# Kernel optimization log

Measured on AMD Instinct MI355X. Metric: run time of the kernel, lower is better.

Reference implementation:

```python
import jax, jax.numpy as jnp
import numpy as np

B, C, H, W = 8, 256, 128, 128
G = 32            # n_groups
CPG = C // G      # channels per group = 8
K = 3             # adaptive spatial kernel and final conv kernel
OUT = 256         # out_channels of final conv
EPS = 1e-5
DN = ('NCHW', 'OIHW', 'NCHW')


def setup_inputs() -> dict:
    key = jax.random.key(0)
    ks = jax.random.split(key, 6)
    x = jax.random.normal(ks[0], (B, C, H, W), jnp.float32)
    w_spatial = jax.random.normal(ks[1], (B, C, CPG, K, K), jnp.float32) * 0.05
    w_pointwise = jax.random.normal(ks[2], (B, C, CPG, 1, 1), jnp.float32) * 0.05
    bias = jax.random.normal(ks[3], (B, C), jnp.float32) * 0.05
    # learned params of the final (static) conv
    conv_w = jax.random.normal(ks[4], (OUT, C, K, K), jnp.float32) * 0.05
    conv_b = jax.random.normal(ks[5], (OUT,), jnp.float32) * 0.05
    return {'x': x, 'w_spatial': w_spatial, 'w_pointwise': w_pointwise,
            'bias': bias, 'conv_w': conv_w, 'conv_b': conv_b}


def _ada_single(x, ws, wp, b):
    # x: [C,H,W]; ws: [C,CPG,K,K]; wp: [C,CPG,1,1]; b: [C]
    pad = (K - 1) // 2
    xp = jnp.pad(x, ((0, 0), (pad, pad), (pad, pad)), mode='reflect')
    # grouped spatial conv (channel-preserving)
    y = jax.lax.conv_general_dilated(
        xp[None], ws, (1, 1), 'VALID',
        dimension_numbers=DN, feature_group_count=G)[0]      # [C,H,W]
    # grouped 1x1 conv as per-group small matmul
    yg = y.reshape(G, CPG, H, W)
    wg = wp[:, :, 0, 0].reshape(G, CPG, CPG)                 # [G, out/g, in/g]
    z = jnp.einsum('goi,gihw->gohw', wg, yg).reshape(C, H, W)
    return z + b[:, None, None]


def reference(x, w_spatial, w_pointwise, bias, conv_w, conv_b):
    # instance norm (no affine), biased variance as in F.instance_norm
    mean = x.mean(axis=(2, 3), keepdims=True)
    var = x.var(axis=(2, 3), keepdims=True)
    xn = (x - mean) * jax.lax.rsqrt(var + EPS)
    # per-sample adaptive depthwise-separable conv
    y = jax.vmap(_ada_single)(xn, w_spatial, w_pointwise, bias)  # [B,C,H,W]
    # final static conv, reflect padding (ceil,floor) = (1,1) for k=3
    yp = jnp.pad(y, ((0, 0), (0, 0), (1, 1), (1, 1)), mode='reflect')
    out = jax.lax.conv_general_dilated(yp, conv_w, (1, 1), 'VALID',
                                       dimension_numbers=DN)
    return out + conv_b[None, :, None, None]
```

## Files before the change

### kernel.cpp

```cpp
#include <hip/hip_runtime.h>
#include <stdint.h>
#include <stddef.h>


typedef __attribute__((ext_vector_type(8))) short   s16x8;
typedef __attribute__((ext_vector_type(4))) float   f32x4;

#define NB   8
#define NC   256
#define NH   128
#define NW   128
#define NG   32
#define CPG  8
#define NOUT 256
#define HWPLANE (NH*NW)

__device__ __forceinline__ unsigned short f2bf(float f) {
    union { float f; unsigned u; } v; v.f = f;
    unsigned u = v.u;
    u += 0x7fffu + ((u >> 16) & 1u);
    return (unsigned short)(u >> 16);
}

__device__ __forceinline__ int refl128(int i) {
    return i < 0 ? 1 : (i > 127 ? 126 : i);
}

__device__ __forceinline__ void async_load16(const void* g, void* l) {
    __builtin_amdgcn_global_load_lds(
        (const __attribute__((address_space(1))) unsigned int*)g,
        (__attribute__((address_space(3))) unsigned int*)l,
        16, 0, 0);
}

__global__ __launch_bounds__(256) void stats_k(const float* __restrict__ x,
                                               float* __restrict__ stats) {
    int bc = blockIdx.x, t = threadIdx.x;
    const float4* p = (const float4*)(x + (size_t)bc * HWPLANE);
    float s = 0.f, q = 0.f;
#pragma unroll
    for (int k = 0; k < 16; ++k) {
        float4 v = p[k * 256 + t];
        s += v.x + v.y + v.z + v.w;
        q += v.x * v.x + v.y * v.y + v.z * v.z + v.w * v.w;
    }
    __shared__ float ss[256], sq[256];
    ss[t] = s; sq[t] = q;
    __syncthreads();
    for (int o = 128; o > 0; o >>= 1) {
        if (t < o) { ss[t] += ss[t + o]; sq[t] += sq[t + o]; }
        __syncthreads();
    }
    if (t == 0) {
        float mean = ss[0] * (1.f / HWPLANE);
        float var  = sq[0] * (1.f / HWPLANE) - mean * mean;
        stats[bc * 2]     = mean;
        stats[bc * 2 + 1] = rsqrtf(var + 1e-5f);
    }
}

__global__ __launch_bounds__(256) void weff_k(const float* __restrict__ wsp,
                                              const float* __restrict__ wpw,
                                              float* __restrict__ weff) {
    int tid = blockIdx.x * 256 + threadIdx.x;
    int oc = tid & 7;
    int q  = tid >> 3;
    int t  = q % 9;
    int q2 = q / 9;
    int ic = q2 & 7;
    int bg = q2 >> 3;
    float acc = 0.f;
#pragma unroll
    for (int j = 0; j < 8; ++j)
        acc += wpw[(bg * 8 + oc) * 8 + j] * wsp[((bg * 8 + j) * 8 + ic) * 9 + t];
    weff[(size_t)((bg * 8 + ic) * 9 + t) * 8 + oc] = acc;
}

__global__ __launch_bounds__(256) void repack_k(const float* __restrict__ cw,
                                                unsigned short* __restrict__ wtT) {
    int tid = blockIdx.x * 256 + threadIdx.x;
    int c = tid & 255;
    int o = (tid >> 8) & 255;
    int t = tid >> 16;
    float v = cw[(size_t)(o * NC + c) * 9 + t];
    wtT[((size_t)t * NOUT + o) * NC + c] = f2bf(v);
}

__global__ __launch_bounds__(256) void ada_k(const float* __restrict__ x,
                                             const float* __restrict__ stats,
                                             const float* __restrict__ weff,
                                             const float* __restrict__ bias,
                                             unsigned short* __restrict__ z) {
    __shared__ float sx[CPG][10][NW];
    const int bx = blockIdx.x;
    const int ht = bx & 15;
    const int g  = (bx >> 4) & 31;
    const int b  = bx >> 9;
    const int h0 = ht * 8;

#pragma unroll
    for (int it = 0; it < 10; ++it) {
        int p   = it * 256 + threadIdx.x;
        int ic  = p / 320;
        int rem = p - ic * 320;
        int row = rem >> 5;
        int w4  = rem & 31;
        int cg  = g * 8 + ic;
        float mean = stats[(b * NC + cg) * 2];
        float rstd = stats[(b * NC + cg) * 2 + 1];
        int rr = refl128(h0 - 1 + row);
        const float4* xp4 = (const float4*)(x + (size_t)(b * NC + cg) * HWPLANE + rr * NW);
        float4 v = xp4[w4];
        float4 n = { (v.x - mean) * rstd, (v.y - mean) * rstd,
                     (v.z - mean) * rstd, (v.w - mean) * rstd };
        *(float4*)&sx[ic][row][w4 * 4] = n;
    }
    __syncthreads();

    const int w  = threadIdx.x & 127;
    const int hq = threadIdx.x >> 7;

    const float* wbase = weff + (size_t)(b * NG + g) * 576;
    const float* bp    = bias + b * NC + g * 8;

    float acc[4][8];
#pragma unroll
    for (int r = 0; r < 4; ++r)
#pragma unroll
        for (int oc = 0; oc < 8; ++oc) acc[r][oc] = bp[oc];

#pragma unroll
    for (int ic = 0; ic < CPG; ++ic) {
#pragma unroll
        for (int dw = 0; dw < 3; ++dw) {
            int wc = w + dw - 1;
            wc = wc < 0 ? 1 : (wc > 127 ? 126 : wc);
            float xr[6];
#pragma unroll
            for (int rr = 0; rr < 6; ++rr) xr[rr] = sx[ic][hq * 4 + rr][wc];
#pragma unroll
            for (int dh = 0; dh < 3; ++dh) {
                const float* wv = wbase + (ic * 9 + dh * 3 + dw) * 8;
#pragma unroll
                for (int r = 0; r < 4; ++r)
#pragma unroll
                    for (int oc = 0; oc < 8; ++oc)
                        acc[r][oc] += wv[oc] * xr[r + dh];
            }
        }
    }

#pragma unroll
    for (int r = 0; r < 4; ++r) {
        int h = h0 + hq * 4 + r;
        unsigned short ob[8];
#pragma unroll
        for (int oc = 0; oc < 8; ++oc) ob[oc] = f2bf(acc[r][oc]);
        uint4 pk;
        pk.x = (unsigned)ob[0] | ((unsigned)ob[1] << 16);
        pk.y = (unsigned)ob[2] | ((unsigned)ob[3] << 16);
        pk.z = (unsigned)ob[4] | ((unsigned)ob[5] << 16);
        pk.w = (unsigned)ob[6] | ((unsigned)ob[7] << 16);
        *(uint4*)(z + (size_t)(((b * NG + g) * NH + h) * NW + w) * 8) = pk;
    }
}

__global__ __launch_bounds__(256, 3) void final_k(const unsigned short* __restrict__ z,
                                                  const unsigned short* __restrict__ wtT,
                                                  const float* __restrict__ cb,
                                                  float* __restrict__ out) {
    __shared__ s16x8 sAv[1024];
    __shared__ s16x8 sBv[2][1024];

    const int id = blockIdx.x;
    const int b  = id & 7;
    const int jb = id >> 3;
    const int nb = jb & 1;
    const int h  = jb >> 1;

    const int tid  = threadIdx.x;
    const int wv   = tid >> 6;
    const int lane = tid & 63;
    const int l15  = lane & 15;
    const int quad = lane >> 4;
    const int mo   = (wv & 1) << 6;
    const int nol  = (wv >> 1) << 6;
    const int n0   = (nb << 7) + nol;

    int srcB[4], ldsoff[4];
#pragma unroll
    for (int it = 0; it < 4; ++it) {
        int ch  = it * 256 + tid;
        int row = ch >> 3, cp = ch & 7;
        srcB[it]   = row * 512 + ((cp ^ (row & 7)) << 4);
        ldsoff[it] = it * 256 + wv * 64;
    }

    int srcA[4];
#pragma unroll
    for (int it = 0; it < 4; ++it) {
        int ch = it * 256 + tid;
        int gq = ch >> 7, wslot = ch & 127;
        srcA[it] = gq * 262144 + ((wslot ^ (gq & 7)) << 4);
    }

    int aoff[3][4][2];
#pragma unroll
    for (int dw = 0; dw < 3; ++dw)
#pragma unroll
        for (int i = 0; i < 4; ++i) {
            int w_ = refl128(mo + 16 * i + l15 + dw - 1);
#pragma unroll
            for (int kk = 0; kk < 2; ++kk) {
                int gq = kk * 4 + quad;
                aoff[dw][i][kk] = gq * 128 + (w_ ^ (gq & 7));
            }
        }
    int boff[4][2];
#pragma unroll
    for (int j = 0; j < 4; ++j) {
        int oc_l = nol + 16 * j + l15;
#pragma unroll
        for (int kk = 0; kk < 2; ++kk)
            boff[j][kk] = oc_l * 8 + ((kk * 4 + quad) ^ (oc_l & 7));
    }

    const char* zb = (const char*)z + (size_t)b * (NG * NH * NW * CPG * 2);
    const char* zr[3];
#pragma unroll
    for (int dh = 0; dh < 3; ++dh)
        zr[dh] = zb + (size_t)refl128(h + dh - 1) * (NW * CPG * 2);
    const char* wt = (const char*)wtT + nb * 65536;

    auto stageA = [&](const char* g) {
#pragma unroll
        for (int it = 0; it < 4; ++it)
            async_load16(g + srcA[it], (void*)(sAv + ldsoff[it]));
    };
    auto stageB = [&](const char* g, int bsel) {
#pragma unroll
        for (int it = 0; it < 4; ++it)
            async_load16(g + srcB[it], (void*)(sBv[bsel] + ldsoff[it]));
    };

    f32x4 acc[4][4] = {};

    auto compute = [&](const int (&ao)[4][2], int bsel) {
        const s16x8* bbase = sBv[bsel];
#pragma unroll
        for (int kk = 0; kk < 2; ++kk) {
            s16x8 av[4], bv[4];
#pragma unroll
            for (int i = 0; i < 4; ++i) av[i] = sAv[ao[i][kk]];
#pragma unroll
            for (int j = 0; j < 4; ++j) bv[j] = bbase[boff[j][kk]];
#pragma unroll
            for (int i = 0; i < 4; ++i)
#pragma unroll
                for (int j = 0; j < 4; ++j)
                    acc[i][j] = __builtin_amdgcn_mfma_f32_16x16x32_bf16(
                        av[i], bv[j], acc[i][j], 0, 0, 0);
        }
    };

    int buf = 0;
    stageA(zr[0]);
    stageB(wt, 0);
    __syncthreads();

    for (int sc = 0; sc < 12; ++sc) {
        const int dh = sc >> 2, kc = sc & 3;
        const char* bt = wt + (size_t)(dh * 3) * 131072 + kc * 128;
        stageB(bt + 131072, buf ^ 1);
        compute(aoff[0], buf);
        __syncthreads(); buf ^= 1;
        stageB(bt + 262144, buf ^ 1);
        compute(aoff[1], buf);
        __syncthreads(); buf ^= 1;
        compute(aoff[2], buf);
        __syncthreads();
        if (sc < 11) {
            const int sn = sc + 1, dhn = sn >> 2, kcn = sn & 3;
            stageA(zr[dhn] + (size_t)kcn * 2097152);
            stageB(wt + (size_t)(dhn * 3) * 131072 + kcn * 128, buf ^ 1);
            __syncthreads();
        }
        buf ^= 1;
    }

#pragma unroll
    for (int j = 0; j < 4; ++j) {
        int oc = n0 + 16 * j + l15;
        float bvl = cb[oc];
#pragma unroll
        for (int i = 0; i < 4; ++i) {
            int w0 = mo + 16 * i + quad * 4;
            float* dst = out + (((size_t)(b * NOUT + oc) * NH + h) * NW + w0);
            f32x4 v = acc[i][j];
            float4 o4 = { v[0] + bvl, v[1] + bvl, v[2] + bvl, v[3] + bvl };
            *(float4*)dst = o4;
        }
    }
}

extern "C" void kernel_launch(void* const* d_in, const int* in_sizes, int n_in,
                              void* d_out, int out_size, void* d_ws, size_t ws_size,
                              hipStream_t stream) {
    const float* x   = (const float*)d_in[0];
    const float* wsp = (const float*)d_in[1];
    const float* wpw = (const float*)d_in[2];
    const float* bia = (const float*)d_in[3];
    const float* cw  = (const float*)d_in[4];
    const float* cb  = (const float*)d_in[5];
    float* out = (float*)d_out;

    char* ws = (char*)d_ws;
    float*          stats = (float*)ws;
    float*          weff  = (float*)(ws + 16384);
    unsigned short* wtT   = (unsigned short*)(ws + 606208);
    unsigned short* z     = (unsigned short*)(ws + 1785856);

    stats_k <<<NB * NC, 256, 0, stream>>>(x, stats);
    weff_k  <<<576,     256, 0, stream>>>(wsp, wpw, weff);
    repack_k<<<2304,    256, 0, stream>>>(cw, wtT);
    ada_k   <<<NB * NG * (NH / 8), 256, 0, stream>>>(x, stats, weff, bia, z);
    final_k <<<NB * NH * 2,  256, 0, stream>>>(z, wtT, cb, out);
}
```

Baseline: 428.2 us.

## Load conv weights directly to registers and double-buffer input tile in LDS

The final conv kernel stops staging weight (B) tiles through shared memory. Each wave now reads its B fragments from global memory straight into registers, while the activation (A) tile is double-buffered in LDS so the next tile loads during compute. This cuts the barriers per chunk from several to one. The A LDS layout changes to a w-major swizzle, MFMA sections get raised scheduling priority, and the occupancy hint in launch_bounds is dropped. The cost is more register pressure and repeated global/L2 reads of weights per wave, which may lower occupancy.

After: 611.0 us. +42.7%, slower.

```diff
diff --git a/kernel.cpp b/kernel.cpp
--- a/kernel.cpp
+++ b/kernel.cpp
@@ -165,12 +165,11 @@
     }
 }
 
-__global__ __launch_bounds__(256, 3) void final_k(const unsigned short* __restrict__ z,
-                                                  const unsigned short* __restrict__ wtT,
-                                                  const float* __restrict__ cb,
-                                                  float* __restrict__ out) {
-    __shared__ s16x8 sAv[1024];
-    __shared__ s16x8 sBv[2][1024];
+__global__ __launch_bounds__(256) void final_k(const unsigned short* __restrict__ z,
+                                               const unsigned short* __restrict__ wtT,
+                                               const float* __restrict__ cb,
+                                               float* __restrict__ out) {
+    __shared__ s16x8 sAv[2][1024];
 
     const int id = blockIdx.x;
     const int b  = id & 7;
@@ -187,21 +186,14 @@
     const int nol  = (wv >> 1) << 6;
     const int n0   = (nb << 7) + nol;
 
-    int srcB[4], ldsoff[4];
-#pragma unroll
-    for (int it = 0; it < 4; ++it) {
-        int ch  = it * 256 + tid;
-        int row = ch >> 3, cp = ch & 7;
-        srcB[it]   = row * 512 + ((cp ^ (row & 7)) << 4);
-        ldsoff[it] = it * 256 + wv * 64;
-    }
-
-    int srcA[4];
+    int srcA[4], ldsoff[4];
 #pragma unroll
     for (int it = 0; it < 4; ++it) {
         int ch = it * 256 + tid;
-        int gq = ch >> 7, wslot = ch & 127;
-        srcA[it] = gq * 262144 + ((wslot ^ (gq & 7)) << 4);
+        int w_ = ch >> 3, s = ch & 7;
+        int gq = s ^ (w_ & 7);
+        srcA[it]   = gq * 262144 + w_ * 16;
+        ldsoff[it] = it * 256 + wv * 64;
     }
 
     int aoff[3][4][2];
@@ -213,16 +205,17 @@
 #pragma unroll
             for (int kk = 0; kk < 2; ++kk) {
                 int gq = kk * 4 + quad;
-                aoff[dw][i][kk] = gq * 128 + (w_ ^ (gq & 7));
+                aoff[dw][i][kk] = w_ * 8 + (gq ^ (w_ & 7));
             }
         }
-    int boff[4][2];
+
+    int boffr[4][2];
 #pragma unroll
     for (int j = 0; j < 4; ++j) {
         int oc_l = nol + 16 * j + l15;
 #pragma unroll
         for (int kk = 0; kk < 2; ++kk)
-            boff[j][kk] = oc_l * 8 + ((kk * 4 + quad) ^ (oc_l & 7));
+            boffr[j][kk] = oc_l * 512 + (kk * 4 + quad) * 16;
     }
 
     const char* zb = (const char*)z + (size_t)b * (NG * NH * NW * CPG * 2);
@@ -232,59 +225,59 @@
         zr[dh] = zb + (size_t)refl128(h + dh - 1) * (NW * CPG * 2);
     const char* wt = (const char*)wtT + nb * 65536;
 
-    auto stageA = [&](const char* g) {
+    auto stageA = [&](const char* g, int sel) {
 #pragma unroll
         for (int it = 0; it < 4; ++it)
-            async_load16(g + srcA[it], (void*)(sAv + ldsoff[it]));
+            async_load16(g + srcA[it], (void*)(sAv[sel] + ldsoff[it]));
     };
-    auto stageB = [&](const char* g, int bsel) {
-#pragma unroll
-        for (int it = 0; it < 4; ++it)
-            async_load16(g + srcB[it], (void*)(sBv[bsel] + ldsoff[it]));
+    auto loadB = [&](const char* bt, s16x8 (&bv)[4][2]) {
+#pragma unroll
+        for (int j = 0; j < 4; ++j)
+#pragma unroll
+            for (int kk = 0; kk < 2; ++kk)
+                bv[j][kk] = *(const s16x8*)(bt + boffr[j][kk]);
     };
 
     f32x4 acc[4][4] = {};
 
-    auto compute = [&](const int (&ao)[4][2], int bsel) {
-        const s16x8* bbase = sBv[bsel];
+    auto compute = [&](const int (&ao)[4][2], const s16x8 (&bv)[4][2], int sel) {
+        const s16x8* abase = sAv[sel];
+        __builtin_amdgcn_s_setprio(1);
 #pragma unroll
         for (int kk = 0; kk < 2; ++kk) {
-            s16x8 av[4], bv[4];
-#pragma unroll
-            for (int i = 0; i < 4; ++i) av[i] = sAv[ao[i][kk]];
-#pragma unroll
-            for (int j = 0; j < 4; ++j) bv[j] = bbase[boff[j][kk]];
+            s16x8 av[4];
+#pragma unroll
+            for (int i = 0; i < 4; ++i) av[i] = abase[ao[i][kk]];
 #pragma unroll
             for (int i = 0; i < 4; ++i)
 #pragma unroll
                 for (int j = 0; j < 4; ++j)
                     acc[i][j] = __builtin_amdgcn_mfma_f32_16x16x32_bf16(
-                        av[i], bv[j], acc[i][j], 0, 0, 0);
-        }
+                        av[i], bv[j][kk], acc[i][j], 0, 0, 0);
+        }
+        __builtin_amdgcn_s_setprio(0);
     };
 
     int buf = 0;
-    stageA(zr[0]);
-    stageB(wt, 0);
+    stageA(zr[0], 0);
     __syncthreads();
 
     for (int sc = 0; sc < 12; ++sc) {
         const int dh = sc >> 2, kc = sc & 3;
-        const char* bt = wt + (size_t)(dh * 3) * 131072 + kc * 128;
-        stageB(bt + 131072, buf ^ 1);
-        compute(aoff[0], buf);
-        __syncthreads(); buf ^= 1;
-        stageB(bt + 262144, buf ^ 1);
-        compute(aoff[1], buf);
-        __syncthreads(); buf ^= 1;
-        compute(aoff[2], buf);
+        const char* bt0 = wt + (size_t)(dh * 3) * 131072 + kc * 128;
+
+        s16x8 bvA[4][2], bvB[4][2];
+        loadB(bt0, bvA);
+        if (sc < 11) {
+            const int sn = sc + 1;
+            stageA(zr[sn >> 2] + (size_t)(sn & 3) * 2097152, buf ^ 1);
+        }
+        loadB(bt0 + 131072, bvB);
+        compute(aoff[0], bvA, buf);
+        loadB(bt0 + 262144, bvA);
+        compute(aoff[1], bvB, buf);
+        compute(aoff[2], bvA, buf);
         __syncthreads();
-        if (sc < 11) {
-            const int sn = sc + 1, dhn = sn >> 2, kcn = sn & 3;
-            stageA(zr[dhn] + (size_t)kcn * 2097152);
-            stageB(wt + (size_t)(dhn * 3) * 131072 + kcn * 128, buf ^ 1);
-            __syncthreads();
-        }
         buf ^= 1;
     }
 
```

## Compute two output rows per block in final conv to share weight tiles

Applied to the files above, without the earlier changes.

The final conv kernel now uses 512-thread blocks that each produce two output rows instead of one. Staged weight (B) tiles in LDS are shared across both rows, which halves weight traffic per output, and the A tile is restaged as two rows with a new swizzle. MFMA sections are also wrapped in s_setprio to favour compute waves. The cost is a larger LDS footprint, half as many blocks, and the loss of the explicit 3-block occupancy hint.

Result: slower. 496.8 us (+16.0%).

```diff
diff --git a/kernel.cpp b/kernel.cpp
--- a/kernel.cpp
+++ b/kernel.cpp
@@ -165,43 +165,49 @@
     }
 }
 
-__global__ __launch_bounds__(256, 3) void final_k(const unsigned short* __restrict__ z,
-                                                  const unsigned short* __restrict__ wtT,
-                                                  const float* __restrict__ cb,
-                                                  float* __restrict__ out) {
-    __shared__ s16x8 sAv[1024];
+__global__ __launch_bounds__(512) void final_k(const unsigned short* __restrict__ z,
+                                               const unsigned short* __restrict__ wtT,
+                                               const float* __restrict__ cb,
+                                               float* __restrict__ out) {
+    __shared__ s16x8 sAv[2048];
     __shared__ s16x8 sBv[2][1024];
 
     const int id = blockIdx.x;
     const int b  = id & 7;
     const int jb = id >> 3;
     const int nb = jb & 1;
-    const int h  = jb >> 1;
+    const int ht = jb >> 1;
+    const int h0 = ht * 2;
 
     const int tid  = threadIdx.x;
     const int wv   = tid >> 6;
     const int lane = tid & 63;
     const int l15  = lane & 15;
     const int quad = lane >> 4;
-    const int mo   = (wv & 1) << 6;
-    const int nol  = (wv >> 1) << 6;
+    const int wsub = wv & 3;
+    const int hrow = wsub >> 1;
+    const int wo   = (wsub & 1) << 6;
+    const int nol  = (wv >> 2) << 6;
     const int n0   = (nb << 7) + nol;
 
-    int srcB[4], ldsoff[4];
+    int srcA[4], ldsA[4];
 #pragma unroll
     for (int it = 0; it < 4; ++it) {
-        int ch  = it * 256 + tid;
-        int row = ch >> 3, cp = ch & 7;
-        srcB[it]   = row * 512 + ((cp ^ (row & 7)) << 4);
-        ldsoff[it] = it * 256 + wv * 64;
-    }
-
-    int srcA[4];
-#pragma unroll
-    for (int it = 0; it < 4; ++it) {
-        int ch = it * 256 + tid;
-        int gq = ch >> 7, wslot = ch & 127;
-        srcA[it] = gq * 262144 + ((wslot ^ (gq & 7)) << 4);
+        int ch = it * 512 + tid;
+        int cw = (ch >> 3) & 127;
+        int s  = ch & 7;
+        int gq = s ^ (cw & 7);
+        srcA[it] = gq * 262144 + cw * 16;
+        ldsA[it] = it * 512 + wv * 64;
+    }
+
+    int srcB[2], ldsB[2];
+#pragma unroll
+    for (int it = 0; it < 2; ++it) {
+        int ch = it * 512 + tid;
+        int oc = ch >> 3, cp = ch & 7;
+        srcB[it] = oc * 512 + ((cp ^ (oc & 7)) << 4);
+        ldsB[it] = it * 512 + wv * 64;
     }
 
     int aoff[3][4][2];
@@ -209,11 +215,11 @@
     for (int dw = 0; dw < 3; ++dw)
 #pragma unroll
         for (int i = 0; i < 4; ++i) {
-            int w_ = refl128(mo + 16 * i + l15 + dw - 1);
+            int w_ = refl128(wo + 16 * i + l15 + dw - 1);
 #pragma unroll
             for (int kk = 0; kk < 2; ++kk) {
                 int gq = kk * 4 + quad;
-                aoff[dw][i][kk] = gq * 128 + (w_ ^ (gq & 7));
+                aoff[dw][i][kk] = hrow * 1024 + w_ * 8 + (gq ^ (w_ & 7));
             }
         }
     int boff[4][2];
@@ -226,27 +232,29 @@
     }
 
     const char* zb = (const char*)z + (size_t)b * (NG * NH * NW * CPG * 2);
-    const char* zr[3];
-#pragma unroll
-    for (int dh = 0; dh < 3; ++dh)
-        zr[dh] = zb + (size_t)refl128(h + dh - 1) * (NW * CPG * 2);
+    const char* zrow[4];
+#pragma unroll
+    for (int r = 0; r < 4; ++r)
+        zrow[r] = zb + (size_t)refl128(h0 + r - 1) * (NW * CPG * 2);
     const char* wt = (const char*)wtT + nb * 65536;
 
-    auto stageA = [&](const char* g) {
-#pragma unroll
-        for (int it = 0; it < 4; ++it)
-            async_load16(g + srcA[it], (void*)(sAv + ldsoff[it]));
+    auto stageA = [&](const char* rp0, const char* rp1) {
+        async_load16(rp0 + srcA[0], (void*)(sAv + ldsA[0]));
+        async_load16(rp0 + srcA[1], (void*)(sAv + ldsA[1]));
+        async_load16(rp1 + srcA[2], (void*)(sAv + ldsA[2]));
+        async_load16(rp1 + srcA[3], (void*)(sAv + ldsA[3]));
     };
     auto stageB = [&](const char* g, int bsel) {
 #pragma unroll
-        for (int it = 0; it < 4; ++it)
-            async_load16(g + srcB[it], (void*)(sBv[bsel] + ldsoff[it]));
+        for (int it = 0; it < 2; ++it)
+            async_load16(g + srcB[it], (void*)(sBv[bsel] + ldsB[it]));
     };
 
     f32x4 acc[4][4] = {};
 
     auto compute = [&](const int (&ao)[4][2], int bsel) {
         const s16x8* bbase = sBv[bsel];
+        __builtin_amdgcn_s_setprio(1);
 #pragma unroll
         for (int kk = 0; kk < 2; ++kk) {
             s16x8 av[4], bv[4];
@@ -261,10 +269,11 @@
                     acc[i][j] = __builtin_amdgcn_mfma_f32_16x16x32_bf16(
                         av[i], bv[j], acc[i][j], 0, 0, 0);
         }
+        __builtin_amdgcn_s_setprio(0);
     };
 
     int buf = 0;
-    stageA(zr[0]);
+    stageA(zrow[0], zrow[1]);
     stageB(wt, 0);
     __syncthreads();
 
@@ -281,20 +290,22 @@
         __syncthreads();
         if (sc < 11) {
             const int sn = sc + 1, dhn = sn >> 2, kcn = sn & 3;
-            stageA(zr[dhn] + (size_t)kcn * 2097152);
+            const size_t ko = (size_t)kcn * 2097152;
+            stageA(zrow[dhn] + ko, zrow[dhn + 1] + ko);
             stageB(wt + (size_t)(dhn * 3) * 131072 + kcn * 128, buf ^ 1);
             __syncthreads();
         }
         buf ^= 1;
     }
 
+    const int h = h0 + hrow;
 #pragma unroll
     for (int j = 0; j < 4; ++j) {
         int oc = n0 + 16 * j + l15;
         float bvl = cb[oc];
 #pragma unroll
         for (int i = 0; i < 4; ++i) {
-            int w0 = mo + 16 * i + quad * 4;
+            int w0 = wo + 16 * i + quad * 4;
             float* dst = out + (((size_t)(b * NOUT + oc) * NH + h) * NW + w0);
             f32x4 v = acc[i][j];
             float4 o4 = { v[0] + bvl, v[1] + bvl, v[2] + bvl, v[3] + bvl };
@@ -324,5 +335,5 @@
     weff_k  <<<576,     256, 0, stream>>>(wsp, wpw, weff);
     repack_k<<<2304,    256, 0, stream>>>(cw, wtT);
     ada_k   <<<NB * NG * (NH / 8), 256, 0, stream>>>(x, stats, weff, bia, z);
-    final_k <<<NB * NH * 2,  256, 0, stream>>>(z, wtT, cb, out);
-}
+    final_k <<<NB * NH * 2 / 2, 512, 0, stream>>>(z, wtT, cb, out);
+}
```

## Compute adaptive grouped conv with bf16 MFMA and change z layout swizzle

Applied to the files above, without the earlier changes.

The adaptive grouped 3x3+1x1 conv moves from scalar fp32 FMAs to bf16 MFMA 16x16x32. The fused effective weights are pre-packed into per-lane fragments, with 9 taps padded to 12 and 8 output channels padded to 16. Each block now normalizes a 34-row bf16 tile for 32 output rows, and the final conv's A-load swizzle is changed to match the new LDS addressing. This cuts the VALU cost of the ada stage but wastes half the MFMA outputs and lowers the normalized input to bf16 before the first conv. It also drops the occupancy hint on final_k.

Measured after the change: 447.9 us. +4.6%, slower.

```diff
diff --git a/kernel.cpp b/kernel.cpp
--- a/kernel.cpp
+++ b/kernel.cpp
@@ -59,21 +59,41 @@
     }
 }
 
-__global__ __launch_bounds__(256) void weff_k(const float* __restrict__ wsp,
-                                              const float* __restrict__ wpw,
-                                              float* __restrict__ weff) {
+__global__ __launch_bounds__(256) void wfrag_k(const float* __restrict__ wsp,
+                                               const float* __restrict__ wpw,
+                                               const float* __restrict__ bias,
+                                               unsigned short* __restrict__ wfrag,
+                                               float* __restrict__ bias16) {
     int tid = blockIdx.x * 256 + threadIdx.x;
-    int oc = tid & 7;
-    int q  = tid >> 3;
-    int t  = q % 9;
-    int q2 = q / 9;
-    int ic = q2 & 7;
-    int bg = q2 >> 3;
-    float acc = 0.f;
-#pragma unroll
-    for (int j = 0; j < 8; ++j)
-        acc += wpw[(bg * 8 + oc) * 8 + j] * wsp[((bg * 8 + j) * 8 + ic) * 9 + t];
-    weff[(size_t)((bg * 8 + ic) * 9 + t) * 8 + oc] = acc;
+    if (tid < 49152) {
+        int lane = tid & 63;
+        int kw   = (tid >> 6) % 3;
+        int bg   = tid / 192;
+        int oc   = lane & 15;
+        int tap  = kw * 4 + (lane >> 4);
+        unsigned short fr[8];
+#pragma unroll
+        for (int e = 0; e < 8; ++e) {
+            float v = 0.f;
+            if (tap < 9 && oc < 8) {
+#pragma unroll
+                for (int j = 0; j < 8; ++j)
+                    v += wpw[(bg * 8 + oc) * 8 + j] *
+                         wsp[((bg * 8 + j) * 8 + e) * 9 + tap];
+            }
+            fr[e] = f2bf(v);
+        }
+        uint4 pk;
+        pk.x = (unsigned)fr[0] | ((unsigned)fr[1] << 16);
+        pk.y = (unsigned)fr[2] | ((unsigned)fr[3] << 16);
+        pk.z = (unsigned)fr[4] | ((unsigned)fr[5] << 16);
+        pk.w = (unsigned)fr[6] | ((unsigned)fr[7] << 16);
+        *(uint4*)(wfrag + (size_t)((bg * 3 + kw) * 64 + lane) * 8) = pk;
+    } else {
+        int t2 = tid - 49152;
+        int bg = t2 >> 4, j = t2 & 15;
+        bias16[bg * 16 + j] = (j < 8) ? bias[bg * 8 + j] : 0.f;
+    }
 }
 
 __global__ __launch_bounds__(256) void repack_k(const float* __restrict__ cw,
@@ -88,87 +108,95 @@
 
 __global__ __launch_bounds__(256) void ada_k(const float* __restrict__ x,
                                              const float* __restrict__ stats,
-                                             const float* __restrict__ weff,
-                                             const float* __restrict__ bias,
+                                             const unsigned short* __restrict__ wfrag,
+                                             const float* __restrict__ bias16,
                                              unsigned short* __restrict__ z) {
-    __shared__ float sx[CPG][10][NW];
-    const int bx = blockIdx.x;
-    const int ht = bx & 15;
-    const int g  = (bx >> 4) & 31;
-    const int b  = bx >> 9;
-    const int h0 = ht * 8;
-
-#pragma unroll
-    for (int it = 0; it < 10; ++it) {
-        int p   = it * 256 + threadIdx.x;
-        int ic  = p / 320;
-        int rem = p - ic * 320;
-        int row = rem >> 5;
-        int w4  = rem & 31;
-        int cg  = g * 8 + ic;
-        float mean = stats[(b * NC + cg) * 2];
-        float rstd = stats[(b * NC + cg) * 2 + 1];
-        int rr = refl128(h0 - 1 + row);
-        const float4* xp4 = (const float4*)(x + (size_t)(b * NC + cg) * HWPLANE + rr * NW);
-        float4 v = xp4[w4];
-        float4 n = { (v.x - mean) * rstd, (v.y - mean) * rstd,
-                     (v.z - mean) * rstd, (v.w - mean) * rstd };
-        *(float4*)&sx[ic][row][w4 * 4] = n;
+    __shared__ s16x8 tile[34 * 128];
+    const int id = blockIdx.x;
+    const int b  = id & 7;
+    const int g  = (id >> 3) & 31;
+    const int q  = id >> 8;
+    const int bg = b * 32 + g;
+    const int h0 = q * 32;
+
+    const int tid  = threadIdx.x;
+    const int lane = tid & 63;
+    const int wv   = tid >> 6;
+    const int l15  = lane & 15;
+    const int quad = lane >> 4;
+
+    float mean[8], rstd[8];
+#pragma unroll
+    for (int ic = 0; ic < 8; ++ic) {
+        mean[ic] = stats[(bg * 8 + ic) * 2];
+        rstd[ic] = stats[(bg * 8 + ic) * 2 + 1];
+    }
+
+    const float* xg = x + (size_t)bg * 8 * HWPLANE;
+#pragma unroll
+    for (int it = 0; it < 17; ++it) {
+        int slot = it * 256 + tid;
+        int row  = slot >> 7;
+        int w    = slot & 127;
+        int gr   = refl128(h0 - 1 + row);
+        const float* xp = xg + gr * NW + w;
+        unsigned short u[8];
+#pragma unroll
+        for (int ic = 0; ic < 8; ++ic)
+            u[ic] = f2bf((xp[(size_t)ic * HWPLANE] - mean[ic]) * rstd[ic]);
+        uint4 pk;
+        pk.x = (unsigned)u[0] | ((unsigned)u[1] << 16);
+        pk.y = (unsigned)u[2] | ((unsigned)u[3] << 16);
+        pk.z = (unsigned)u[4] | ((unsigned)u[5] << 16);
+        pk.w = (unsigned)u[6] | ((unsigned)u[7] << 16);
+        *(uint4*)&tile[slot] = pk;
     }
     __syncthreads();
 
-    const int w  = threadIdx.x & 127;
-    const int hq = threadIdx.x >> 7;
-
-    const float* wbase = weff + (size_t)(b * NG + g) * 576;
-    const float* bp    = bias + b * NC + g * 8;
-
-    float acc[4][8];
-#pragma unroll
-    for (int r = 0; r < 4; ++r)
-#pragma unroll
-        for (int oc = 0; oc < 8; ++oc) acc[r][oc] = bp[oc];
-
-#pragma unroll
-    for (int ic = 0; ic < CPG; ++ic) {
-#pragma unroll
-        for (int dw = 0; dw < 3; ++dw) {
-            int wc = w + dw - 1;
-            wc = wc < 0 ? 1 : (wc > 127 ? 126 : wc);
-            float xr[6];
-#pragma unroll
-            for (int rr = 0; rr < 6; ++rr) xr[rr] = sx[ic][hq * 4 + rr][wc];
-#pragma unroll
-            for (int dh = 0; dh < 3; ++dh) {
-                const float* wv = wbase + (ic * 9 + dh * 3 + dw) * 8;
-#pragma unroll
-                for (int r = 0; r < 4; ++r)
-#pragma unroll
-                    for (int oc = 0; oc < 8; ++oc)
-                        acc[r][oc] += wv[oc] * xr[r + dh];
-            }
-        }
-    }
-
-#pragma unroll
-    for (int r = 0; r < 4; ++r) {
-        int h = h0 + hq * 4 + r;
-        unsigned short ob[8];
-#pragma unroll
-        for (int oc = 0; oc < 8; ++oc) ob[oc] = f2bf(acc[r][oc]);
-        uint4 pk;
-        pk.x = (unsigned)ob[0] | ((unsigned)ob[1] << 16);
-        pk.y = (unsigned)ob[2] | ((unsigned)ob[3] << 16);
-        pk.z = (unsigned)ob[4] | ((unsigned)ob[5] << 16);
-        pk.w = (unsigned)ob[6] | ((unsigned)ob[7] << 16);
-        *(uint4*)(z + (size_t)(((b * NG + g) * NH + h) * NW + w) * 8) = pk;
-    }
-}
-
-__global__ __launch_bounds__(256, 3) void final_k(const unsigned short* __restrict__ z,
-                                                  const unsigned short* __restrict__ wtT,
-                                                  const float* __restrict__ cb,
-                                                  float* __restrict__ out) {
+    s16x8 wf[3];
+#pragma unroll
+    for (int kw = 0; kw < 3; ++kw)
+        wf[kw] = *(const s16x8*)(wfrag + (size_t)((bg * 3 + kw) * 64 + lane) * 8);
+    float4 bv = *(const float4*)(bias16 + bg * 16 + quad * 4);
+
+    int dhA[3], dwm[3];
+#pragma unroll
+    for (int kw = 0; kw < 3; ++kw) {
+        int tap = kw * 4 + quad;
+        if (tap < 9) { dhA[kw] = tap / 3; dwm[kw] = tap % 3 - 1; }
+        else         { dhA[kw] = 0;       dwm[kw] = 0; }
+    }
+
+#pragma unroll 2
+    for (int i = 0; i < 64; ++i) {
+        int pb = wv * 64 + i;
+        int ro = pb >> 3;
+        int w0 = (pb & 7) * 16;
+        f32x4 acc = {};
+#pragma unroll
+        for (int kw = 0; kw < 3; ++kw) {
+            int wr = refl128(w0 + l15 + dwm[kw]);
+            s16x8 xf = tile[(ro + dhA[kw]) * 128 + wr];
+            acc = __builtin_amdgcn_mfma_f32_16x16x32_bf16(wf[kw], xf, acc, 0, 0, 0);
+        }
+        unsigned short o0 = f2bf(acc[0] + bv.x);
+        unsigned short o1 = f2bf(acc[1] + bv.y);
+        unsigned short o2 = f2bf(acc[2] + bv.z);
+        unsigned short o3 = f2bf(acc[3] + bv.w);
+        if (lane < 32) {
+            uint2 pk2 = { (unsigned)o0 | ((unsigned)o1 << 16),
+                          (unsigned)o2 | ((unsigned)o3 << 16) };
+            unsigned short* zp = z + ((size_t)(bg * NH + h0 + ro) * NW + w0 + l15) * 8
+                                   + quad * 4;
+            *(uint2*)zp = pk2;
+        }
+    }
+}
+
+__global__ __launch_bounds__(256) void final_k(const unsigned short* __restrict__ z,
+                                               const unsigned short* __restrict__ wtT,
+                                               const float* __restrict__ cb,
+                                               float* __restrict__ out) {
     __shared__ s16x8 sAv[1024];
     __shared__ s16x8 sBv[2][1024];
 
@@ -187,21 +215,21 @@
     const int nol  = (wv >> 1) << 6;
     const int n0   = (nb << 7) + nol;
 
-    int srcB[4], ldsoff[4];
+    int srcA[4], ldsoff[4];
+#pragma unroll
+    for (int it = 0; it < 4; ++it) {
+        int ch = it * 256 + tid;
+        int w_ = ch >> 3, s = ch & 7;
+        int gq = s ^ (w_ & 7);
+        srcA[it]   = gq * 262144 + w_ * 16;
+        ldsoff[it] = it * 256 + wv * 64;
+    }
+    int srcB[4];
 #pragma unroll
     for (int it = 0; it < 4; ++it) {
         int ch  = it * 256 + tid;
         int row = ch >> 3, cp = ch & 7;
-        srcB[it]   = row * 512 + ((cp ^ (row & 7)) << 4);
-        ldsoff[it] = it * 256 + wv * 64;
-    }
-
-    int srcA[4];
-#pragma unroll
-    for (int it = 0; it < 4; ++it) {
-        int ch = it * 256 + tid;
-        int gq = ch >> 7, wslot = ch & 127;
-        srcA[it] = gq * 262144 + ((wslot ^ (gq & 7)) << 4);
+        srcB[it] = row * 512 + ((cp ^ (row & 7)) << 4);
     }
 
     int aoff[3][4][2];
@@ -213,7 +241,7 @@
 #pragma unroll
             for (int kk = 0; kk < 2; ++kk) {
                 int gq = kk * 4 + quad;
-                aoff[dw][i][kk] = gq * 128 + (w_ ^ (gq & 7));
+                aoff[dw][i][kk] = w_ * 8 + (gq ^ (w_ & 7));
             }
         }
     int boff[4][2];
@@ -315,14 +343,15 @@
     float* out = (float*)d_out;
 
     char* ws = (char*)d_ws;
-    float*          stats = (float*)ws;
-    float*          weff  = (float*)(ws + 16384);
-    unsigned short* wtT   = (unsigned short*)(ws + 606208);
-    unsigned short* z     = (unsigned short*)(ws + 1785856);
+    float*          stats  = (float*)ws;
+    unsigned short* wfrag  = (unsigned short*)(ws + 16384);
+    float*          bias16 = (float*)(ws + 802816);
+    unsigned short* wtT    = (unsigned short*)(ws + 819200);
+    unsigned short* z      = (unsigned short*)(ws + 1998848);
 
     stats_k <<<NB * NC, 256, 0, stream>>>(x, stats);
-    weff_k  <<<576,     256, 0, stream>>>(wsp, wpw, weff);
+    wfrag_k <<<208,     256, 0, stream>>>(wsp, wpw, bia, wfrag, bias16);
     repack_k<<<2304,    256, 0, stream>>>(cw, wtT);
-    ada_k   <<<NB * NG * (NH / 8), 256, 0, stream>>>(x, stats, weff, bia, z);
-    final_k <<<NB * NH * 2,  256, 0, stream>>>(z, wtT, cb, out);
-}
+    ada_k   <<<NB * NG * 4, 256, 0, stream>>>(x, stats, wfrag, bias16, z);
+    final_k <<<NB * NH * 2, 256, 0, stream>>>(z, wtT, cb, out);
+}
```
